# Performance work log

Hardware: AMD Instinct MI355X
Metric: run time of the kernel (lower is better)

The kernel has to match this reference:

```python
import jax, jax.numpy as jnp
import numpy as np

NUM_CLASSES = 6

def _weight_matrix(num_classes, weight_type='quadratic'):
    i = jnp.arange(num_classes, dtype=jnp.float32)
    d = jnp.abs(i[:, None] - i[None, :])
    if weight_type == 'linear':
        return d
    elif weight_type == 'quadratic':
        return d ** 2
    else:
        raise ValueError("weight_type must be 'linear' or 'quadratic'")

def setup_inputs() -> dict:
    key = jax.random.key(0)
    k1, k2 = jax.random.split(key)
    N = 4_000_000
    y_pred = jax.random.normal(k1, (N, NUM_CLASSES), dtype=jnp.float32)
    y_true = jax.random.randint(k2, (N,), 0, NUM_CLASSES, dtype=jnp.int64)
    return {"y_pred": y_pred, "y_true": y_true}

def reference(y_pred, y_true):
    C = NUM_CLASSES
    t = y_true.reshape(-1).astype(jnp.int32)
    probs = jax.nn.softmax(y_pred, axis=1)
    p = jnp.argmax(probs, axis=1).astype(jnp.int32)
    # histograms over classes (equivalent to torch.histc with bins=C, min=0, max=C-1)
    hist_true = jnp.bincount(t, length=C).astype(jnp.float32)
    hist_pred = jnp.bincount(p, length=C).astype(jnp.float32)
    # confusion matrix in one fused scatter-add pass (replaces the Python loop)
    flat = t * C + p  # [N]
    confusion = jnp.bincount(flat, length=C * C).astype(jnp.float32).reshape(C, C)
    confusion = confusion / confusion.sum()
    expected = jnp.outer(hist_true, hist_pred)
    expected = expected / expected.sum()
    W = _weight_matrix(C, 'quadratic')
    kappa = 1.0 - (W * confusion).sum() / (W * expected).sum()
    return kappa
```

## Files before the change

kernel.cpp:

```cpp
#include <hip/hip_runtime.h>


#define NC 6
#define NBINS 36
#define BLOCK 256
#define WPB (BLOCK / 64)
#define GRID 1024
#define CHUNK 64
#define SEGS 16
#define FIN_THREADS (NBINS * SEGS)

typedef float f4 __attribute__((ext_vector_type(4)));

__device__ __forceinline__ f4 ld_stream_b128(const f4* p) {
    f4 r;
    asm volatile("global_load_dwordx4 %0, %1, off sc1 nt"
                 : "=v"(r) : "v"(p) : "memory");
    return r;
}
__device__ __forceinline__ unsigned long long ld_stream_b64(
    const unsigned long long* p) {
    unsigned long long r;
    asm volatile("global_load_dwordx2 %0, %1, off sc1 nt"
                 : "=v"(r) : "v"(p) : "memory");
    return r;
}

__global__ __launch_bounds__(BLOCK) void kappa_count(
    const f4* __restrict__ yp4, const unsigned long long* __restrict__ yt2,
    const float* __restrict__ yp, const int* __restrict__ yt,
    unsigned int* __restrict__ gconf, int npairs, int N) {
    __shared__ f4 stage[WPB][3 * CHUNK];
    __shared__ unsigned int sconf[WPB][NBINS];
    const int tid = threadIdx.x;
    const int w = tid >> 6;
    const int L = tid & 63;
    if (tid < WPB * NBINS) ((unsigned int*)sconf)[tid] = 0u;
    __syncthreads();

    unsigned int* my = sconf[w];
    f4* st = stage[w];

    const int nchunks = npairs / CHUNK;
    const int gwaves = GRID * WPB;
    for (int c = blockIdx.x * WPB + w; c < nchunks; c += gwaves) {
        const f4 g0 = ld_stream_b128(&yp4[c * 3 * CHUNK + L]);
        const f4 g1 = ld_stream_b128(&yp4[c * 3 * CHUNK + 64 + L]);
        const f4 g2 = ld_stream_b128(&yp4[c * 3 * CHUNK + 128 + L]);
        const unsigned long long tt = ld_stream_b64(&yt2[c * CHUNK + L]);
        asm volatile("s_waitcnt vmcnt(0)" ::: "memory");
        __builtin_amdgcn_sched_barrier(0);
        st[L] = g0;
        st[64 + L] = g1;
        st[128 + L] = g2;
        __threadfence_block();
        const f4 a = st[3 * L];
        const f4 b = st[3 * L + 1];
        const f4 d = st[3 * L + 2];
        const int t0 = (int)(tt & 0xffffffffull);
        const int t1 = (int)(tt >> 32);

        float m = a.x; int p = 0;
        if (a.y > m) { m = a.y; p = 1; }
        if (a.z > m) { m = a.z; p = 2; }
        if (a.w > m) { m = a.w; p = 3; }
        if (b.x > m) { m = b.x; p = 4; }
        if (b.y > m) { m = b.y; p = 5; }
        atomicAdd(&my[t0 * NC + p], 1u);

        m = b.z; p = 0;
        if (b.w > m) { m = b.w; p = 1; }
        if (d.x > m) { m = d.x; p = 2; }
        if (d.y > m) { m = d.y; p = 3; }
        if (d.z > m) { m = d.z; p = 4; }
        if (d.w > m) { m = d.w; p = 5; }
        atomicAdd(&my[t1 * NC + p], 1u);
    }

    const int rem0 = nchunks * CHUNK;
    if (blockIdx.x == 0 && tid < npairs - rem0) {
        const int i = rem0 + tid;
        const f4 a = yp4[3 * i];
        const f4 b = yp4[3 * i + 1];
        const f4 d = yp4[3 * i + 2];
        const unsigned long long tt = yt2[i];
        const int t0 = (int)(tt & 0xffffffffull);
        const int t1 = (int)(tt >> 32);
        float m = a.x; int p = 0;
        if (a.y > m) { m = a.y; p = 1; }
        if (a.z > m) { m = a.z; p = 2; }
        if (a.w > m) { m = a.w; p = 3; }
        if (b.x > m) { m = b.x; p = 4; }
        if (b.y > m) { m = b.y; p = 5; }
        atomicAdd(&my[t0 * NC + p], 1u);
        m = b.z; p = 0;
        if (b.w > m) { m = b.w; p = 1; }
        if (d.x > m) { m = d.x; p = 2; }
        if (d.y > m) { m = d.y; p = 3; }
        if (d.z > m) { m = d.z; p = 4; }
        if (d.w > m) { m = d.w; p = 5; }
        atomicAdd(&my[t1 * NC + p], 1u);
    }

    if ((N & 1) && blockIdx.x == 0 && tid == 0) {
        const int r = N - 1;
        float m = yp[r * NC]; int p = 0;
        #pragma unroll
        for (int j = 1; j < NC; ++j) {
            const float v = yp[r * NC + j];
            if (v > m) { m = v; p = j; }
        }
        atomicAdd(&my[yt[r] * NC + p], 1u);
    }

    __syncthreads();
    if (tid < NBINS) {
        unsigned int s = 0;
        #pragma unroll
        for (int k = 0; k < WPB; ++k) s += sconf[k][tid];
        gconf[blockIdx.x * NBINS + tid] = s;
    }
}

__global__ void kappa_final_kernel(const unsigned int* __restrict__ gconf,
                                   float* __restrict__ out, long long N) {
    __shared__ unsigned int part[SEGS][NBINS];
    __shared__ unsigned int conf_s[NBINS];
    const int tid = threadIdx.x;
    if (tid < FIN_THREADS) {
        const int bin = tid % NBINS;
        const int seg = tid / NBINS;
        unsigned int s = 0;
        const int b0 = seg * (GRID / SEGS);
        #pragma unroll 8
        for (int b = b0; b < b0 + GRID / SEGS; ++b) s += gconf[b * NBINS + bin];
        part[seg][bin] = s;
    }
    __syncthreads();
    if (tid < NBINS) {
        unsigned int tot = 0;
        #pragma unroll
        for (int s2 = 0; s2 < SEGS; ++s2) tot += part[s2][tid];
        conf_s[tid] = tot;
    }
    __syncthreads();
    if (tid == 0) {
        long long conf[NBINS], ht[NC], hp[NC];
        #pragma unroll
        for (int i = 0; i < NC; ++i) { ht[i] = 0; hp[i] = 0; }
        #pragma unroll
        for (int k = 0; k < NBINS; ++k) conf[k] = (long long)conf_s[k];

        long long num = 0;
        #pragma unroll
        for (int i = 0; i < NC; ++i)
            #pragma unroll
            for (int j = 0; j < NC; ++j) {
                const long long w = (long long)(i - j) * (i - j);
                num += w * conf[i * NC + j];
                ht[i] += conf[i * NC + j];
                hp[j] += conf[i * NC + j];
            }
        long long den = 0;
        #pragma unroll
        for (int i = 0; i < NC; ++i)
            #pragma unroll
            for (int j = 0; j < NC; ++j)
                den += (long long)(i - j) * (i - j) * ht[i] * hp[j];

        out[0] = (float)(1.0 - ((double)num * (double)N) / (double)den);
    }
}

extern "C" void kernel_launch(void* const* d_in, const int* in_sizes, int n_in,
                              void* d_out, int out_size, void* d_ws, size_t ws_size,
                              hipStream_t stream) {
    const float* yp = (const float*)d_in[0];
    const int* yt = (const int*)d_in[1];
    const int N = in_sizes[1];
    unsigned int* gconf = (unsigned int*)d_ws;

    const int npairs = N / 2;
    kappa_count<<<GRID, BLOCK, 0, stream>>>(
        (const f4*)yp, (const unsigned long long*)yt, yp, yt, gconf, npairs, N);
    kappa_final_kernel<<<1, FIN_THREADS, 0, stream>>>(gconf, (float*)d_out,
                                                      (long long)N);
}
```

Baseline: 145.0 us.

## Double per-wave chunk size and transpose partial histogram layout for vectorized final reduce

Each wave now loads two 64-pair groups per iteration (six 16-byte loads plus two label loads) before waiting, which doubles the bytes in flight per loop trip. The LDS staging fence is replaced with an explicit lgkmcnt wait. Per-block partial histograms are stored bin-major so the final kernel can sum them with coalesced uint4 loads. In exchange, each wave uses more registers, fewer chunks remain to spread across waves (possible tail imbalance), and the final kernel hardcodes GRID=1024.

```diff
diff --git a/kernel.cpp b/kernel.cpp
--- a/kernel.cpp
+++ b/kernel.cpp
@@ -6,9 +6,8 @@
 #define BLOCK 256
 #define WPB (BLOCK / 64)
 #define GRID 1024
-#define CHUNK 64
-#define SEGS 16
-#define FIN_THREADS (NBINS * SEGS)
+#define CHUNK 128
+#define FIN_THREADS (NBINS * 16)
 
 typedef float f4 __attribute__((ext_vector_type(4)));
 
@@ -24,6 +23,18 @@
     asm volatile("global_load_dwordx2 %0, %1, off sc1 nt"
                  : "=v"(r) : "v"(p) : "memory");
     return r;
+}
+
+__device__ __forceinline__ void bump(unsigned int* __restrict__ my, int t,
+                                     float e0, float e1, float e2,
+                                     float e3, float e4, float e5) {
+    float m = e0; int p = 0;
+    if (e1 > m) { m = e1; p = 1; }
+    if (e2 > m) { m = e2; p = 2; }
+    if (e3 > m) { m = e3; p = 3; }
+    if (e4 > m) { m = e4; p = 4; }
+    if (e5 > m) { m = e5; p = 5; }
+    atomicAdd(&my[t * NC + p], 1u);
 }
 
 __global__ __launch_bounds__(BLOCK) void kappa_count(
@@ -47,34 +58,35 @@
         const f4 g0 = ld_stream_b128(&yp4[c * 3 * CHUNK + L]);
         const f4 g1 = ld_stream_b128(&yp4[c * 3 * CHUNK + 64 + L]);
         const f4 g2 = ld_stream_b128(&yp4[c * 3 * CHUNK + 128 + L]);
-        const unsigned long long tt = ld_stream_b64(&yt2[c * CHUNK + L]);
+        const f4 g3 = ld_stream_b128(&yp4[c * 3 * CHUNK + 192 + L]);
+        const f4 g4 = ld_stream_b128(&yp4[c * 3 * CHUNK + 256 + L]);
+        const f4 g5 = ld_stream_b128(&yp4[c * 3 * CHUNK + 320 + L]);
+        const unsigned long long t0v = ld_stream_b64(&yt2[c * CHUNK + L]);
+        const unsigned long long t1v = ld_stream_b64(&yt2[c * CHUNK + 64 + L]);
         asm volatile("s_waitcnt vmcnt(0)" ::: "memory");
         __builtin_amdgcn_sched_barrier(0);
         st[L] = g0;
         st[64 + L] = g1;
         st[128 + L] = g2;
-        __threadfence_block();
-        const f4 a = st[3 * L];
-        const f4 b = st[3 * L + 1];
-        const f4 d = st[3 * L + 2];
-        const int t0 = (int)(tt & 0xffffffffull);
-        const int t1 = (int)(tt >> 32);
-
-        float m = a.x; int p = 0;
-        if (a.y > m) { m = a.y; p = 1; }
-        if (a.z > m) { m = a.z; p = 2; }
-        if (a.w > m) { m = a.w; p = 3; }
-        if (b.x > m) { m = b.x; p = 4; }
-        if (b.y > m) { m = b.y; p = 5; }
-        atomicAdd(&my[t0 * NC + p], 1u);
-
-        m = b.z; p = 0;
-        if (b.w > m) { m = b.w; p = 1; }
-        if (d.x > m) { m = d.x; p = 2; }
-        if (d.y > m) { m = d.y; p = 3; }
-        if (d.z > m) { m = d.z; p = 4; }
-        if (d.w > m) { m = d.w; p = 5; }
-        atomicAdd(&my[t1 * NC + p], 1u);
+        st[192 + L] = g3;
+        st[256 + L] = g4;
+        st[320 + L] = g5;
+        asm volatile("s_waitcnt lgkmcnt(0)" ::: "memory");
+        __builtin_amdgcn_sched_barrier(0);
+        {
+            const f4 a = st[3 * L];
+            const f4 b = st[3 * L + 1];
+            const f4 d = st[3 * L + 2];
+            bump(my, (int)(t0v & 0xffffffffull), a.x, a.y, a.z, a.w, b.x, b.y);
+            bump(my, (int)(t0v >> 32),           b.z, b.w, d.x, d.y, d.z, d.w);
+        }
+        {
+            const f4 a = st[192 + 3 * L];
+            const f4 b = st[192 + 3 * L + 1];
+            const f4 d = st[192 + 3 * L + 2];
+            bump(my, (int)(t1v & 0xffffffffull), a.x, a.y, a.z, a.w, b.x, b.y);
+            bump(my, (int)(t1v >> 32),           b.z, b.w, d.x, d.y, d.z, d.w);
+        }
     }
 
     const int rem0 = nchunks * CHUNK;
@@ -84,22 +96,8 @@
         const f4 b = yp4[3 * i + 1];
         const f4 d = yp4[3 * i + 2];
         const unsigned long long tt = yt2[i];
-        const int t0 = (int)(tt & 0xffffffffull);
-        const int t1 = (int)(tt >> 32);
-        float m = a.x; int p = 0;
-        if (a.y > m) { m = a.y; p = 1; }
-        if (a.z > m) { m = a.z; p = 2; }
-        if (a.w > m) { m = a.w; p = 3; }
-        if (b.x > m) { m = b.x; p = 4; }
-        if (b.y > m) { m = b.y; p = 5; }
-        atomicAdd(&my[t0 * NC + p], 1u);
-        m = b.z; p = 0;
-        if (b.w > m) { m = b.w; p = 1; }
-        if (d.x > m) { m = d.x; p = 2; }
-        if (d.y > m) { m = d.y; p = 3; }
-        if (d.z > m) { m = d.z; p = 4; }
-        if (d.w > m) { m = d.w; p = 5; }
-        atomicAdd(&my[t1 * NC + p], 1u);
+        bump(my, (int)(tt & 0xffffffffull), a.x, a.y, a.z, a.w, b.x, b.y);
+        bump(my, (int)(tt >> 32),           b.z, b.w, d.x, d.y, d.z, d.w);
     }
 
     if ((N & 1) && blockIdx.x == 0 && tid == 0) {
@@ -118,29 +116,32 @@
         unsigned int s = 0;
         #pragma unroll
         for (int k = 0; k < WPB; ++k) s += sconf[k][tid];
-        gconf[blockIdx.x * NBINS + tid] = s;
+        gconf[tid * GRID + blockIdx.x] = s;
     }
 }
 
 __global__ void kappa_final_kernel(const unsigned int* __restrict__ gconf,
                                    float* __restrict__ out, long long N) {
-    __shared__ unsigned int part[SEGS][NBINS];
+    __shared__ unsigned int part[NBINS][16];
     __shared__ unsigned int conf_s[NBINS];
     const int tid = threadIdx.x;
-    if (tid < FIN_THREADS) {
-        const int bin = tid % NBINS;
-        const int seg = tid / NBINS;
+    {
+        const int bin = tid >> 4;
+        const int seg = tid & 15;
+        const uint4* g4 = (const uint4*)gconf;
         unsigned int s = 0;
-        const int b0 = seg * (GRID / SEGS);
-        #pragma unroll 8
-        for (int b = b0; b < b0 + GRID / SEGS; ++b) s += gconf[b * NBINS + bin];
-        part[seg][bin] = s;
+        #pragma unroll
+        for (int j = 0; j < 16; ++j) {
+            const uint4 v = g4[bin * 256 + seg * 16 + j];
+            s += v.x + v.y + v.z + v.w;
+        }
+        part[bin][seg] = s;
     }
     __syncthreads();
     if (tid < NBINS) {
         unsigned int tot = 0;
         #pragma unroll
-        for (int s2 = 0; s2 < SEGS; ++s2) tot += part[s2][tid];
+        for (int s2 = 0; s2 < 16; ++s2) tot += part[tid][s2];
         conf_s[tid] = tot;
     }
     __syncthreads();
```

Measured after the change: 148.9 us. +2.7%, slower.
